# Performance work log

Hardware: AMD Instinct MI355X
Metric: run time of the kernel (lower is better)

## Reference

```python
import jax, jax.numpy as jnp
import numpy as np

VOCAB = 5000; EMB = 300; AUDIO = 74; HID = 128
D1 = 16; D2 = 16; DIM = D1 * D2
UNITS = 128; CELL = 64; OUT = 1
B = 32; S = 32
NGRAMS = (1, 3)


def _lstm(x, w_ih, w_hh, b_ih, b_hh):
    # PyTorch LSTMCell semantics, gate order i, f, g, o
    Bb = x.shape[0]; H = w_hh.shape[1]
    def step(carry, xt):
        h, c = carry
        gates = xt @ w_ih.T + h @ w_hh.T + b_ih + b_hh
        i, f, g, o = jnp.split(gates, 4, axis=-1)
        c = jax.nn.sigmoid(f) * c + jax.nn.sigmoid(i) * jnp.tanh(g)
        h = jax.nn.sigmoid(o) * jnp.tanh(c)
        return (h, c), h
    init = (jnp.zeros((Bb, H), x.dtype), jnp.zeros((Bb, H), x.dtype))
    _, hs = jax.lax.scan(step, init, jnp.swapaxes(x, 0, 1))
    return jnp.swapaxes(hs, 0, 1)  # (B, S, H)


def _windows(x, n):
    # zero-padded n-gram windows: (B, S, d) -> (B, S, n, d)
    xp = jnp.pad(x, ((0, 0), (0, n - 1), (0, 0)))
    s = x.shape[1]
    return jnp.stack([xp[:, k:k + s, :] for k in range(n)], axis=2)


def setup_inputs() -> dict:
    key = jax.random.key(0)
    ks = jax.random.split(key, 26)
    g = lambda i, shape, sc=0.05: jax.random.normal(ks[i], shape, dtype=jnp.float32) * sc
    return dict(
        word_indexes=jax.random.randint(ks[0], (B, S), 0, VOCAB),
        audio=jax.random.normal(ks[1], (B, S, AUDIO), dtype=jnp.float32),
        lookup_table=g(2, (VOCAB, EMB), 0.5),
        phase_tab0=g(3, (VOCAB, D1), 3.14),
        phase_tab1=g(4, (VOCAB, D2), 3.14),
        w_ih=g(5, (4 * HID, EMB)), w_hh=g(6, (4 * HID, HID)),
        b_ih=g(7, (4 * HID,)), b_hh=g(8, (4 * HID,)),
        w_lin=g(9, (D1, HID)), b_lin=g(10, (D1,)),
        w1=g(11, (D2, AUDIO)), b1=g(12, (D2,)),
        w2=g(13, (D2, D2)), b2=g(14, (D2,)),
        w3=g(15, (D2, D2)), b3=g(16, (D2,)),
        modality_weights=jnp.zeros((2,), jnp.float32),
        meas_r=g(17, (UNITS, DIM), 0.5), meas_i=g(18, (UNITS, DIM), 0.5),
        fw1=g(19, (CELL, UNITS)), fb1=g(20, (CELL,)),
        fw2=g(21, (CELL, CELL)), fb2=g(22, (CELL,)),
        fw3=g(23, (OUT, CELL)), fb3=jnp.zeros((OUT,), jnp.float32),
    )


def reference(word_indexes, audio, lookup_table, phase_tab0, phase_tab1,
              w_ih, w_hh, b_ih, b_hh, w_lin, b_lin,
              w1, b1, w2, b2, w3, b3,
              modality_weights, meas_r, meas_i,
              fw1, fb1, fw2, fb2, fw3, fb3):
    eps = 1e-10
    # amplitude subnets (dropout rates are 0 / eval mode)
    text = lookup_table[word_indexes]                      # (B,S,EMB)
    h = _lstm(text, w_ih, w_hh, b_ih, b_hh)
    amp0 = h @ w_lin.T + b_lin                             # (B,S,D1)
    a = jax.nn.relu(audio @ w1.T + b1)
    a = jax.nn.relu(a @ w2.T + b2)
    amp1 = jax.nn.relu(a @ w3.T + b3)                      # (B,S,D2)
    ph0 = phase_tab0[word_indexes]
    ph1 = phase_tab1[word_indexes]

    def branch(amp, ph):
        norm = jnp.linalg.norm(amp, axis=-1, keepdims=True)
        ampn = amp / (norm + eps)
        return norm, ampn * jnp.cos(ph), ampn * jnp.sin(ph)

    n0, r0, i0 = branch(amp0, ph0)
    n1, r1, i1 = branch(amp1, ph1)
    mw = jax.nn.softmax(modality_weights)
    weight = mw[0] * n0 + mw[1] * n1                       # (B,S,1)

    # sequential complex tensor product across modalities,
    # starting from (real=1, imag=1) as in the original code
    tpr = r0 - i0
    tpi = r0 + i0
    real = jnp.einsum('bsi,bsj->bsij', tpr, r1) - jnp.einsum('bsi,bsj->bsij', tpi, i1)
    imag = jnp.einsum('bsi,bsj->bsij', tpr, i1) + jnp.einsum('bsi,bsj->bsij', tpi, r1)
    real = real.reshape(B, S, DIM)
    imag = imag.reshape(B, S, DIM)

    # measurement kernel: unit-norm complex vectors
    kn = jnp.sqrt(jnp.sum(meas_r ** 2 + meas_i ** 2, axis=-1, keepdims=True)) + eps
    vr = meas_r / kn
    vi = meas_i / kn

    probs = []
    for n in NGRAMS:
        wr = _windows(real, n)                             # (B,S,n,DIM)
        wi = _windows(imag, n)
        ww = jax.nn.softmax(_windows(weight, n)[..., 0], axis=-1)  # (B,S,n)
        # complex mixture: rho = sum_n w_n |v_n><v_n|
        rho_r = (jnp.einsum('bsn,bsni,bsnj->bsij', ww, wr, wr)
                 + jnp.einsum('bsn,bsni,bsnj->bsij', ww, wi, wi))
        rho_i = (jnp.einsum('bsn,bsni,bsnj->bsij', ww, wi, wr)
                 - jnp.einsum('bsn,bsni,bsnj->bsij', ww, wr, wi))
        # measurement: Re(v^H rho v) per unit
        m = (jnp.einsum('bsij,ui,uj->bsu', rho_r, vr, vr)
             + jnp.einsum('bsij,ui,uj->bsu', rho_r, vi, vi)
             + jnp.einsum('bsij,ui,uj->bsu', rho_i, vi, vr)
             - jnp.einsum('bsij,ui,uj->bsu', rho_i, vr, vi))
        probs.append(m)
    probs = jnp.concatenate(probs, axis=1)                 # (B, S*len(NGRAMS), UNITS)
    feat = jnp.max(probs, axis=1)                          # 'max' pooling
    y = jax.nn.relu(feat @ fw1.T + fb1)
    y = jax.nn.relu(y @ fw2.T + fb2)
    return y @ fw3.T + fb3                                 # (B, OUT)
```

## Files before the change

### kernel.cpp

```cpp
#include <hip/hip_runtime.h>
#include <math.h>


static constexpr unsigned XW0_OFF  = 0u;
static constexpr unsigned XW1_OFF  = 524288u;
static constexpr unsigned HOUT_OFF = 1048576u;
static constexpr unsigned XMAT_OFF = HOUT_OFF + 131072u;
static constexpr unsigned WT_OFF   = XMAT_OFF + 524288u;
static constexpr unsigned VPP_OFF  = WT_OFF + 1024u;
static constexpr unsigned PP_OFF   = VPP_OFF + 131072u;
static constexpr unsigned PP_HALF  = 262144u;

__global__ __launch_bounds__(256) void k1_xw_gemm(
    const int* __restrict__ widx, const float* __restrict__ lut,
    const float* __restrict__ w_ih, const float* __restrict__ b_ih,
    const float* __restrict__ b_hh,
    const float* __restrict__ mr, const float* __restrict__ mi,
    float* __restrict__ ws)
{
  const int bid = blockIdx.x;
  const int t = threadIdx.x;

  if (bid >= 256) {
    const int u = bid - 256;
    float r  = mr[u * 256 + t];
    float ii = mi[u * 256 + t];
    float sq = r * r + ii * ii;
    #pragma unroll
    for (int off = 1; off < 64; off <<= 1) sq += __shfl_xor(sq, off);
    __shared__ float wsum[4];
    if ((t & 63) == 0) wsum[t >> 6] = sq;
    __syncthreads();
    float tot = wsum[0] + wsum[1] + wsum[2] + wsum[3];
    float inv = 1.0f / (sqrtf(tot) + 1e-10f);
    float vr = r * inv, vi = ii * inv;
    float* vpp = ws + VPP_OFF;
    vpp[(2 * u) * 512 + t]           = vr;
    vpp[(2 * u) * 512 + 256 + t]     = vi;
    vpp[(2 * u + 1) * 512 + t]       = -vi;
    vpp[(2 * u + 1) * 512 + 256 + t] = vr;
    return;
  }

  const int rb = bid & 15, cb = (bid >> 4) & 7, kq = bid >> 7;
  const int R = rb * 64, C = cb * 64;
  const int kbase_g = kq * 152;
  const int ktot = kq ? 148 : 152;

  __shared__ alignas(16) float As[32][68];
  __shared__ alignas(16) float Ws[32][68];

  float acc[4][4] = {};
  const int r0 = (t & 15) * 4, j0 = (t >> 4) * 4;

  for (int kt = 0; kt < 5; ++kt) {
    int kl = ktot - kt * 32; if (kl > 32) kl = 32;
    #pragma unroll
    for (int pass = 0; pass < 2; ++pass) {
      int rr = (t >> 3) + pass * 32;
      int kk4 = (t & 7) * 4;
      float4 av = make_float4(0.f, 0.f, 0.f, 0.f);
      float4 wv = make_float4(0.f, 0.f, 0.f, 0.f);
      if (kk4 < kl) {
        int gk = kbase_g + kt * 32 + kk4;
        int word = widx[R + rr];
        av = *(const float4*)&lut[word * 300 + gk];
        wv = *(const float4*)&w_ih[(C + rr) * 300 + gk];
      }
      As[kk4 + 0][rr] = av.x; As[kk4 + 1][rr] = av.y;
      As[kk4 + 2][rr] = av.z; As[kk4 + 3][rr] = av.w;
      Ws[kk4 + 0][rr] = wv.x; Ws[kk4 + 1][rr] = wv.y;
      Ws[kk4 + 2][rr] = wv.z; Ws[kk4 + 3][rr] = wv.w;
    }
    __syncthreads();
    #pragma unroll
    for (int k = 0; k < 32; ++k) {
      float4 a4 = *(const float4*)&As[k][r0];
      float4 w4 = *(const float4*)&Ws[k][j0];
      float ar[4] = {a4.x, a4.y, a4.z, a4.w};
      float wr[4] = {w4.x, w4.y, w4.z, w4.w};
      #pragma unroll
      for (int i2 = 0; i2 < 4; ++i2)
        #pragma unroll
        for (int j2 = 0; j2 < 4; ++j2)
          acc[i2][j2] = fmaf(ar[i2], wr[j2], acc[i2][j2]);
    }
    __syncthreads();
  }

  float* xw = ws + (kq ? XW1_OFF : XW0_OFF);
  #pragma unroll
  for (int i2 = 0; i2 < 4; ++i2) {
    int row = R + r0 + i2, col = C + j0;
    float4 v = make_float4(acc[i2][0], acc[i2][1], acc[i2][2], acc[i2][3]);
    if (kq == 0) {
      v.x += b_ih[col + 0] + b_hh[col + 0];
      v.y += b_ih[col + 1] + b_hh[col + 1];
      v.z += b_ih[col + 2] + b_hh[col + 2];
      v.w += b_ih[col + 3] + b_hh[col + 3];
    }
    *(float4*)&xw[row * 512 + col] = v;
  }
}

__global__ __launch_bounds__(640, 1) void k2_lstm(
    const float* __restrict__ w_hh, float* __restrict__ ws)
{
  const int b = blockIdx.x;
  const int t = threadIdx.x;
  const int wv = t >> 6;
  const int l  = t & 63;

  __shared__ alignas(16) float part[8][512];
  __shared__ alignas(16) float hbuf[2][128];

  float* hout = ws + HOUT_OFF;
  const float* xw0 = ws + XW0_OFF;
  const float* xw1 = ws + XW1_OFF;

  if (t < 128) hbuf[0][t] = 0.f;

  if (wv < 8) {
    float4 wA[4][4], wB[4][4];
    #pragma unroll
    for (int g = 0; g < 4; ++g) {
      const float* pA = w_hh + (g * 128 + l) * 128 + wv * 16;
      const float* pB = w_hh + (g * 128 + 64 + l) * 128 + wv * 16;
      #pragma unroll
      for (int c = 0; c < 4; ++c) {
        wA[g][c] = *(const float4*)&pA[c * 4];
        wB[g][c] = *(const float4*)&pB[c * 4];
      }
    }
    #pragma unroll
    for (int g = 0; g < 4; ++g)
      #pragma unroll
      for (int c = 0; c < 4; ++c) {
        asm volatile("" : "+v"(wA[g][c].x), "+v"(wA[g][c].y), "+v"(wA[g][c].z), "+v"(wA[g][c].w));
        asm volatile("" : "+v"(wB[g][c].x), "+v"(wB[g][c].y), "+v"(wB[g][c].z), "+v"(wB[g][c].w));
      }
    __syncthreads();
    const float* hbase = &hbuf[0][0];
    for (int s = 0; s < 32; ++s) {
      const float* hb = hbase + (s & 1) * 128 + wv * 16;
      float aA0 = 0.f, aA1 = 0.f, aA2 = 0.f, aA3 = 0.f;
      float aB0 = 0.f, aB1 = 0.f, aB2 = 0.f, aB3 = 0.f;
      #pragma unroll
      for (int c = 0; c < 4; ++c) {
        float4 h4 = *(const float4*)&hb[c * 4];
        aA0 = fmaf(wA[0][c].x, h4.x, fmaf(wA[0][c].y, h4.y, fmaf(wA[0][c].z, h4.z, fmaf(wA[0][c].w, h4.w, aA0))));
        aA1 = fmaf(wA[1][c].x, h4.x, fmaf(wA[1][c].y, h4.y, fmaf(wA[1][c].z, h4.z, fmaf(wA[1][c].w, h4.w, aA1))));
        aA2 = fmaf(wA[2][c].x, h4.x, fmaf(wA[2][c].y, h4.y, fmaf(wA[2][c].z, h4.z, fmaf(wA[2][c].w, h4.w, aA2))));
        aA3 = fmaf(wA[3][c].x, h4.x, fmaf(wA[3][c].y, h4.y, fmaf(wA[3][c].z, h4.z, fmaf(wA[3][c].w, h4.w, aA3))));
        aB0 = fmaf(wB[0][c].x, h4.x, fmaf(wB[0][c].y, h4.y, fmaf(wB[0][c].z, h4.z, fmaf(wB[0][c].w, h4.w, aB0))));
        aB1 = fmaf(wB[1][c].x, h4.x, fmaf(wB[1][c].y, h4.y, fmaf(wB[1][c].z, h4.z, fmaf(wB[1][c].w, h4.w, aB1))));
        aB2 = fmaf(wB[2][c].x, h4.x, fmaf(wB[2][c].y, h4.y, fmaf(wB[2][c].z, h4.z, fmaf(wB[2][c].w, h4.w, aB2))));
        aB3 = fmaf(wB[3][c].x, h4.x, fmaf(wB[3][c].y, h4.y, fmaf(wB[3][c].z, h4.z, fmaf(wB[3][c].w, h4.w, aB3))));
      }
      *(float4*)&part[wv][l * 4]       = make_float4(aA0, aA1, aA2, aA3);
      *(float4*)&part[wv][256 + l * 4] = make_float4(aB0, aB1, aB2, aB3);
      __syncthreads();
      __syncthreads();
    }
  } else {
    const int jj = (wv - 8) * 64 + l;
    float c = 0.f;
    __syncthreads();
    for (int s = 0; s < 32; ++s) {
      const int base = (b * 32 + s) * 512 + jj;
      float x0 = xw0[base +   0] + xw1[base +   0];
      float x1 = xw0[base + 128] + xw1[base + 128];
      float x2 = xw0[base + 256] + xw1[base + 256];
      float x3 = xw0[base + 384] + xw1[base + 384];
      __syncthreads();
      float g0 = x0, g1 = x1, g2 = x2, g3 = x3;
      #pragma unroll
      for (int w = 0; w < 8; ++w) {
        float4 p = *(const float4*)&part[w][jj * 4];
        g0 += p.x; g1 += p.y; g2 += p.z; g3 += p.w;
      }
      float si = 1.f / (1.f + __expf(-g0));
      float sf = 1.f / (1.f + __expf(-g1));
      float tg = 1.f - 2.f / (1.f + __expf(2.f * g2));
      float so = 1.f / (1.f + __expf(-g3));
      c = sf * c + si * tg;
      float tc = 1.f - 2.f / (1.f + __expf(2.f * c));
      float hn = so * tc;
      hbuf[(s + 1) & 1][jj] = hn;
      hout[(b * 32 + s) * 128 + jj] = hn;
      __syncthreads();
    }
  }
}

__global__ __launch_bounds__(256) void k3_mix(
    const int* __restrict__ widx, const float* __restrict__ audio,
    const float* __restrict__ ph0t, const float* __restrict__ ph1t,
    const float* __restrict__ w_lin, const float* __restrict__ b_lin,
    const float* __restrict__ w1, const float* __restrict__ b1,
    const float* __restrict__ w2, const float* __restrict__ b2,
    const float* __restrict__ w3, const float* __restrict__ b3,
    const float* __restrict__ modw, float* __restrict__ ws)
{
  const int bs = blockIdx.x;
  const int t = threadIdx.x;
  __shared__ float amp0[16], a1s[16], a2s[16], amp1[16];
  __shared__ float tpr[16], tpi[16], r1s[16], i1s[16];
  __shared__ float nn[2];

  const float* hrow = ws + HOUT_OFF + bs * 128;
  if (t < 16) {
    float acc = b_lin[t];
    for (int u = 0; u < 128; ++u) acc = fmaf(hrow[u], w_lin[t * 128 + u], acc);
    amp0[t] = acc;
  } else if (t >= 64 && t < 80) {
    int d = t - 64;
    float acc = b1[d];
    for (int k = 0; k < 74; ++k) acc = fmaf(audio[bs * 74 + k], w1[d * 74 + k], acc);
    a1s[d] = fmaxf(acc, 0.f);
  }
  __syncthreads();
  if (t < 16) {
    float acc = b2[t];
    #pragma unroll
    for (int k = 0; k < 16; ++k) acc = fmaf(a1s[k], w2[t * 16 + k], acc);
    a2s[t] = fmaxf(acc, 0.f);
  }
  __syncthreads();
  if (t < 16) {
    float acc = b3[t];
    #pragma unroll
    for (int k = 0; k < 16; ++k) acc = fmaf(a2s[k], w3[t * 16 + k], acc);
    amp1[t] = fmaxf(acc, 0.f);
  }
  __syncthreads();
  if (t == 0) {
    float sq = 0.f;
    #pragma unroll
    for (int d = 0; d < 16; ++d) sq += amp0[d] * amp0[d];
    nn[0] = sqrtf(sq);
  } else if (t == 64) {
    float sq = 0.f;
    #pragma unroll
    for (int d = 0; d < 16; ++d) sq += amp1[d] * amp1[d];
    nn[1] = sqrtf(sq);
  }
  __syncthreads();
  const int word = widx[bs];
  if (t < 16) {
    float k0 = amp0[t] / (nn[0] + 1e-10f);
    float ph = ph0t[word * 16 + t];
    float cc = cosf(ph), ssn = sinf(ph);
    tpr[t] = k0 * (cc - ssn);
    tpi[t] = k0 * (cc + ssn);
  } else if (t >= 64 && t < 80) {
    int d = t - 64;
    float k1 = amp1[d] / (nn[1] + 1e-10f);
    float ph = ph1t[word * 16 + d];
    r1s[d] = k1 * cosf(ph);
    i1s[d] = k1 * sinf(ph);
  } else if (t == 128) {
    float e0 = __expf(modw[0]), e1 = __expf(modw[1]);
    float mw0 = e0 / (e0 + e1);
    ws[WT_OFF + bs] = mw0 * nn[0] + (1.f - mw0) * nn[1];
  }
  __syncthreads();
  const int i2 = t >> 4, j2 = t & 15;
  float rr = tpr[i2] * r1s[j2] - tpi[i2] * i1s[j2];
  float im = tpr[i2] * i1s[j2] + tpi[i2] * r1s[j2];
  float* X = ws + XMAT_OFF;
  X[bs * 512 + t] = rr;
  X[bs * 512 + 256 + t] = im;
}

__global__ __launch_bounds__(256) void k4_meas(float* __restrict__ ws)
{
  const int bid = blockIdx.x, t = threadIdx.x;
  const int rb = bid & 15, cb = (bid >> 4) & 3, kq = bid >> 6;
  const int R = rb * 64, C = cb * 64;
  const float* X = ws + XMAT_OFF;
  const float* V = ws + VPP_OFF;
  __shared__ alignas(16) float Xs[32][68];
  __shared__ alignas(16) float Vs[32][68];
  float acc[4][4] = {};
  const int r0 = (t & 15) * 4, j0 = (t >> 4) * 4;

  for (int kt = 0; kt < 4; ++kt) {
    #pragma unroll
    for (int pass = 0; pass < 2; ++pass) {
      int rr = (t >> 3) + pass * 32;
      int kk4 = (t & 7) * 4;
      int gk = kq * 128 + kt * 32 + kk4;
      float4 xv = *(const float4*)&X[(R + rr) * 512 + gk];
      float4 vv = *(const float4*)&V[(C + rr) * 512 + gk];
      Xs[kk4 + 0][rr] = xv.x; Xs[kk4 + 1][rr] = xv.y;
      Xs[kk4 + 2][rr] = xv.z; Xs[kk4 + 3][rr] = xv.w;
      Vs[kk4 + 0][rr] = vv.x; Vs[kk4 + 1][rr] = vv.y;
      Vs[kk4 + 2][rr] = vv.z; Vs[kk4 + 3][rr] = vv.w;
    }
    __syncthreads();
    #pragma unroll
    for (int k = 0; k < 32; ++k) {
      float4 a4 = *(const float4*)&Xs[k][r0];
      float4 w4 = *(const float4*)&Vs[k][j0];
      float ar[4] = {a4.x, a4.y, a4.z, a4.w};
      float wr[4] = {w4.x, w4.y, w4.z, w4.w};
      #pragma unroll
      for (int i2 = 0; i2 < 4; ++i2)
        #pragma unroll
        for (int j2 = 0; j2 < 4; ++j2)
          acc[i2][j2] = fmaf(ar[i2], wr[j2], acc[i2][j2]);
    }
    __syncthreads();
  }
  float* Pp = ws + PP_OFF + (unsigned)kq * PP_HALF;
  #pragma unroll
  for (int i2 = 0; i2 < 4; ++i2) {
    float4 v = make_float4(acc[i2][0], acc[i2][1], acc[i2][2], acc[i2][3]);
    *(float4*)&Pp[(R + r0 + i2) * 256 + C + j0] = v;
  }
}

__global__ __launch_bounds__(512) void k5_final(
    const float* __restrict__ fw1, const float* __restrict__ fb1,
    const float* __restrict__ fw2, const float* __restrict__ fb2,
    const float* __restrict__ fw3, const float* __restrict__ fb3,
    const float* __restrict__ ws, float* __restrict__ out)
{
  const int b = blockIdx.x, t = threadIdx.x;
  const int u = t & 127, sg = t >> 7;
  __shared__ float ewt[34];
  __shared__ float pl[32][128];
  __shared__ float fred[4][128];
  __shared__ float feat[128], y1[64], y2[64];
  if (t < 32) ewt[t] = __expf(ws[WT_OFF + b * 32 + t]);
  if (t >= 32 && t < 34) ewt[t] = 1.f;
  __syncthreads();

  const float* Pp = ws + PP_OFF;
  #pragma unroll
  for (int i = 0; i < 8; ++i) {
    int s = sg * 8 + i;
    int bs = b * 32 + s;
    float A = 0.f, Bv = 0.f;
    #pragma unroll
    for (int kq = 0; kq < 4; ++kq) {
      A  += Pp[kq * PP_HALF + bs * 256 + 2 * u];
      Bv += Pp[kq * PP_HALF + bs * 256 + 2 * u + 1];
    }
    pl[s][u] = A * A + Bv * Bv;
  }
  __syncthreads();

  float m = -1e30f;
  #pragma unroll
  for (int i = 0; i < 8; ++i) {
    int s = sg * 8 + i;
    float p0 = pl[s][u];
    m = fmaxf(m, p0);
    float e0 = ewt[s], e1 = ewt[s + 1], e2 = ewt[s + 2];
    float num = e0 * p0;
    if (s + 1 < 32) num += e1 * pl[s + 1][u];
    if (s + 2 < 32) num += e2 * pl[s + 2][u];
    m = fmaxf(m, num / (e0 + e1 + e2));
  }
  fred[sg][u] = m;
  __syncthreads();
  if (t < 128)
    feat[t] = fmaxf(fmaxf(fred[0][t], fred[1][t]), fmaxf(fred[2][t], fred[3][t]));
  __syncthreads();
  if (t < 64) {
    float acc = fb1[t];
    for (int k = 0; k < 128; ++k) acc = fmaf(feat[k], fw1[t * 128 + k], acc);
    y1[t] = fmaxf(acc, 0.f);
  }
  __syncthreads();
  if (t < 64) {
    float acc = fb2[t];
    #pragma unroll
    for (int k = 0; k < 64; ++k) acc = fmaf(y1[k], fw2[t * 64 + k], acc);
    y2[t] = fmaxf(acc, 0.f);
  }
  __syncthreads();
  if (t == 0) {
    float acc = fb3[0];
    #pragma unroll
    for (int k = 0; k < 64; ++k) acc = fmaf(y2[k], fw3[k], acc);
    out[b] = acc;
  }
}

extern "C" void kernel_launch(void* const* d_in, const int* in_sizes, int n_in,
                              void* d_out, int out_size, void* d_ws, size_t ws_size,
                              hipStream_t stream) {
  const int*   widx  = (const int*)d_in[0];
  const float* audio = (const float*)d_in[1];
  const float* lut   = (const float*)d_in[2];
  const float* ph0   = (const float*)d_in[3];
  const float* ph1   = (const float*)d_in[4];
  const float* w_ih  = (const float*)d_in[5];
  const float* w_hh  = (const float*)d_in[6];
  const float* b_ih  = (const float*)d_in[7];
  const float* b_hh  = (const float*)d_in[8];
  const float* w_lin = (const float*)d_in[9];
  const float* b_lin = (const float*)d_in[10];
  const float* w1    = (const float*)d_in[11];
  const float* b1    = (const float*)d_in[12];
  const float* w2    = (const float*)d_in[13];
  const float* b2    = (const float*)d_in[14];
  const float* w3    = (const float*)d_in[15];
  const float* b3    = (const float*)d_in[16];
  const float* modw  = (const float*)d_in[17];
  const float* mr    = (const float*)d_in[18];
  const float* mi    = (const float*)d_in[19];
  const float* fw1   = (const float*)d_in[20];
  const float* fb1   = (const float*)d_in[21];
  const float* fw2   = (const float*)d_in[22];
  const float* fb2   = (const float*)d_in[23];
  const float* fw3   = (const float*)d_in[24];
  const float* fb3   = (const float*)d_in[25];
  float* ws  = (float*)d_ws;
  float* out = (float*)d_out;

  k1_xw_gemm<<<dim3(384), dim3(256), 0, stream>>>(widx, lut, w_ih, b_ih, b_hh, mr, mi, ws);
  k2_lstm<<<dim3(32), dim3(640), 0, stream>>>(w_hh, ws);
  k3_mix<<<dim3(1024), dim3(256), 0, stream>>>(widx, audio, ph0, ph1, w_lin, b_lin,
                                               w1, b1, w2, b2, w3, b3, modw, ws);
  k4_meas<<<dim3(256), dim3(256), 0, stream>>>(ws);
  k5_final<<<dim3(32), dim3(512), 0, stream>>>(fw1, fb1, fw2, fb2, fw3, fb3, ws, out);
}
```

Baseline: 181.9 us.

## Fuse per-token mixture computation into LSTM kernel using shared-memory hidden history

Merges the per-token state-preparation kernel into the LSTM kernel. The full hidden-state history now stays in shared memory instead of going through global memory, and each of the 32 blocks then computes amplitudes, phases and the 16x16 complex tensor for its 32 tokens. This removes one kernel launch and the global round trip for the hidden states. In exchange, the mix work runs on only 32 blocks instead of 1024, which reduces parallelism for that phase and raises per-block shared memory use.

```diff
diff --git a/kernel.cpp b/kernel.cpp
--- a/kernel.cpp
+++ b/kernel.cpp
@@ -103,8 +103,15 @@
   }
 }
 
-__global__ __launch_bounds__(640, 1) void k2_lstm(
-    const float* __restrict__ w_hh, float* __restrict__ ws)
+__global__ __launch_bounds__(640, 1) void k2_lstm_mix(
+    const float* __restrict__ w_hh, const int* __restrict__ widx,
+    const float* __restrict__ audio,
+    const float* __restrict__ ph0t, const float* __restrict__ ph1t,
+    const float* __restrict__ w_lin, const float* __restrict__ b_lin,
+    const float* __restrict__ w1, const float* __restrict__ b1,
+    const float* __restrict__ w2, const float* __restrict__ b2,
+    const float* __restrict__ w3, const float* __restrict__ b3,
+    const float* __restrict__ modw, float* __restrict__ ws)
 {
   const int b = blockIdx.x;
   const int t = threadIdx.x;
@@ -112,13 +119,15 @@
   const int l  = t & 63;
 
   __shared__ alignas(16) float part[8][512];
-  __shared__ alignas(16) float hbuf[2][128];
-
-  float* hout = ws + HOUT_OFF;
+  __shared__ alignas(16) float hist[33][128];
+  __shared__ float amp0s[32][17], a1s[32][17], a2s[32][17], amp1s[32][17];
+  __shared__ float tprs[32][17], tpis[32][17], r1ss[32][17], i1ss[32][17];
+  __shared__ float nrm0[32], nrm1[32];
+
   const float* xw0 = ws + XW0_OFF;
   const float* xw1 = ws + XW1_OFF;
 
-  if (t < 128) hbuf[0][t] = 0.f;
+  if (t < 128) hist[0][t] = 0.f;
 
   if (wv < 8) {
     float4 wA[4][4], wB[4][4];
@@ -140,9 +149,8 @@
         asm volatile("" : "+v"(wB[g][c].x), "+v"(wB[g][c].y), "+v"(wB[g][c].z), "+v"(wB[g][c].w));
       }
     __syncthreads();
-    const float* hbase = &hbuf[0][0];
     for (int s = 0; s < 32; ++s) {
-      const float* hb = hbase + (s & 1) * 128 + wv * 16;
+      const float* hb = &hist[s][wv * 16];
       float aA0 = 0.f, aA1 = 0.f, aA2 = 0.f, aA3 = 0.f;
       float aB0 = 0.f, aB1 = 0.f, aB2 = 0.f, aB3 = 0.f;
       #pragma unroll
@@ -185,92 +193,86 @@
       float so = 1.f / (1.f + __expf(-g3));
       c = sf * c + si * tg;
       float tc = 1.f - 2.f / (1.f + __expf(2.f * c));
-      float hn = so * tc;
-      hbuf[(s + 1) & 1][jj] = hn;
-      hout[(b * 32 + s) * 128 + jj] = hn;
+      hist[s + 1][jj] = so * tc;
       __syncthreads();
     }
   }
-}
-
-__global__ __launch_bounds__(256) void k3_mix(
-    const int* __restrict__ widx, const float* __restrict__ audio,
-    const float* __restrict__ ph0t, const float* __restrict__ ph1t,
-    const float* __restrict__ w_lin, const float* __restrict__ b_lin,
-    const float* __restrict__ w1, const float* __restrict__ b1,
-    const float* __restrict__ w2, const float* __restrict__ b2,
-    const float* __restrict__ w3, const float* __restrict__ b3,
-    const float* __restrict__ modw, float* __restrict__ ws)
-{
-  const int bs = blockIdx.x;
-  const int t = threadIdx.x;
-  __shared__ float amp0[16], a1s[16], a2s[16], amp1[16];
-  __shared__ float tpr[16], tpi[16], r1s[16], i1s[16];
-  __shared__ float nn[2];
-
-  const float* hrow = ws + HOUT_OFF + bs * 128;
-  if (t < 16) {
-    float acc = b_lin[t];
-    for (int u = 0; u < 128; ++u) acc = fmaf(hrow[u], w_lin[t * 128 + u], acc);
-    amp0[t] = acc;
-  } else if (t >= 64 && t < 80) {
-    int d = t - 64;
-    float acc = b1[d];
-    for (int k = 0; k < 74; ++k) acc = fmaf(audio[bs * 74 + k], w1[d * 74 + k], acc);
-    a1s[d] = fmaxf(acc, 0.f);
-  }
-  __syncthreads();
-  if (t < 16) {
-    float acc = b2[t];
-    #pragma unroll
-    for (int k = 0; k < 16; ++k) acc = fmaf(a1s[k], w2[t * 16 + k], acc);
-    a2s[t] = fmaxf(acc, 0.f);
-  }
-  __syncthreads();
-  if (t < 16) {
-    float acc = b3[t];
-    #pragma unroll
-    for (int k = 0; k < 16; ++k) acc = fmaf(a2s[k], w3[t * 16 + k], acc);
-    amp1[t] = fmaxf(acc, 0.f);
-  }
-  __syncthreads();
-  if (t == 0) {
+
+  const int word_base = b * 32;
+  if (t < 512) {
+    const int s = t >> 4, d = t & 15;
+    float acc = b_lin[d];
+    const float* wl = w_lin + d * 128;
+    const float* hh = hist[s + 1];
+    for (int u = 0; u < 128; ++u) acc = fmaf(hh[u], wl[u], acc);
+    amp0s[s][d] = acc;
+    float a = b1[d];
+    const float* au = audio + (word_base + s) * 74;
+    const float* w1r = w1 + d * 74;
+    for (int k = 0; k < 74; ++k) a = fmaf(au[k], w1r[k], a);
+    a1s[s][d] = fmaxf(a, 0.f);
+  }
+  __syncthreads();
+  if (t < 512) {
+    const int s = t >> 4, d = t & 15;
+    float a = b2[d];
+    #pragma unroll
+    for (int k = 0; k < 16; ++k) a = fmaf(a1s[s][k], w2[d * 16 + k], a);
+    a2s[s][d] = fmaxf(a, 0.f);
+  }
+  __syncthreads();
+  if (t < 512) {
+    const int s = t >> 4, d = t & 15;
+    float a = b3[d];
+    #pragma unroll
+    for (int k = 0; k < 16; ++k) a = fmaf(a2s[s][k], w3[d * 16 + k], a);
+    amp1s[s][d] = fmaxf(a, 0.f);
+  }
+  __syncthreads();
+  if (t < 32) {
     float sq = 0.f;
     #pragma unroll
-    for (int d = 0; d < 16; ++d) sq += amp0[d] * amp0[d];
-    nn[0] = sqrtf(sq);
-  } else if (t == 64) {
+    for (int d = 0; d < 16; ++d) sq += amp0s[t][d] * amp0s[t][d];
+    nrm0[t] = sqrtf(sq);
+  } else if (t >= 64 && t < 96) {
+    int s = t - 64;
     float sq = 0.f;
     #pragma unroll
-    for (int d = 0; d < 16; ++d) sq += amp1[d] * amp1[d];
-    nn[1] = sqrtf(sq);
-  }
-  __syncthreads();
-  const int word = widx[bs];
-  if (t < 16) {
-    float k0 = amp0[t] / (nn[0] + 1e-10f);
-    float ph = ph0t[word * 16 + t];
-    float cc = cosf(ph), ssn = sinf(ph);
-    tpr[t] = k0 * (cc - ssn);
-    tpi[t] = k0 * (cc + ssn);
-  } else if (t >= 64 && t < 80) {
-    int d = t - 64;
-    float k1 = amp1[d] / (nn[1] + 1e-10f);
-    float ph = ph1t[word * 16 + d];
-    r1s[d] = k1 * cosf(ph);
-    i1s[d] = k1 * sinf(ph);
-  } else if (t == 128) {
+    for (int d = 0; d < 16; ++d) sq += amp1s[s][d] * amp1s[s][d];
+    nrm1[s] = sqrtf(sq);
+  }
+  __syncthreads();
+  if (t < 512) {
+    const int s = t >> 4, d = t & 15;
+    const int word = widx[word_base + s];
+    float k0 = amp0s[s][d] / (nrm0[s] + 1e-10f);
+    float ph = ph0t[word * 16 + d];
+    float cc = cosf(ph), sn = sinf(ph);
+    tprs[s][d] = k0 * (cc - sn);
+    tpis[s][d] = k0 * (cc + sn);
+    float k1v = amp1s[s][d] / (nrm1[s] + 1e-10f);
+    float p1 = ph1t[word * 16 + d];
+    r1ss[s][d] = k1v * cosf(p1);
+    i1ss[s][d] = k1v * sinf(p1);
+  } else if (t >= 512 && t < 544) {
+    int s = t - 512;
     float e0 = __expf(modw[0]), e1 = __expf(modw[1]);
     float mw0 = e0 / (e0 + e1);
-    ws[WT_OFF + bs] = mw0 * nn[0] + (1.f - mw0) * nn[1];
-  }
-  __syncthreads();
-  const int i2 = t >> 4, j2 = t & 15;
-  float rr = tpr[i2] * r1s[j2] - tpi[i2] * i1s[j2];
-  float im = tpr[i2] * i1s[j2] + tpi[i2] * r1s[j2];
-  float* X = ws + XMAT_OFF;
-  X[bs * 512 + t] = rr;
-  X[bs * 512 + 256 + t] = im;
+    ws[WT_OFF + word_base + s] = mw0 * nrm0[s] + (1.f - mw0) * nrm1[s];
+  }
+  __syncthreads();
+  if (t < 512) {
+    float* X = ws + XMAT_OFF;
+    const int c2 = t;
+    const int half = c2 >> 8;
+    const int i2 = (c2 >> 4) & 15, j2 = c2 & 15;
+    for (int s = 0; s < 32; ++s) {
+      float v;
+      if (half == 0) v = tprs[s][i2] * r1ss[s][j2] - tpis[s][i2] * i1ss[s][j2];
+      else           v = tprs[s][i2] * i1ss[s][j2] + tpis[s][i2] * r1ss[s][j2];
+      X[(word_base + s) * 512 + c2] = v;
+    }
+  }
 }
 
 __global__ __launch_bounds__(256) void k4_meas(float* __restrict__ ws)
@@ -423,9 +425,9 @@
   float* out = (float*)d_out;
 
   k1_xw_gemm<<<dim3(384), dim3(256), 0, stream>>>(widx, lut, w_ih, b_ih, b_hh, mr, mi, ws);
-  k2_lstm<<<dim3(32), dim3(640), 0, stream>>>(w_hh, ws);
-  k3_mix<<<dim3(1024), dim3(256), 0, stream>>>(widx, audio, ph0, ph1, w_lin, b_lin,
-                                               w1, b1, w2, b2, w3, b3, modw, ws);
+  k2_lstm_mix<<<dim3(32), dim3(640), 0, stream>>>(w_hh, widx, audio, ph0, ph1,
+                                                  w_lin, b_lin, w1, b1, w2, b2,
+                                                  w3, b3, modw, ws);
   k4_meas<<<dim3(256), dim3(256), 0, stream>>>(ws);
   k5_final<<<dim3(32), dim3(512), 0, stream>>>(fw1, fb1, fw2, fb2, fw3, fb3, ws, out);
 }
```

After: 190.7 us. 4.8% more time.
